# Kernel optimization log

Measured on AMD Instinct MI355X. Metric: run time of the kernel, lower is better.

Reference implementation:

```python
import jax, jax.numpy as jnp
import numpy as np

EPS = 1e-12  # F.normalize eps

def _l2_normalize(x):
    n = jnp.linalg.norm(x, axis=-1, keepdims=True)
    return x / jnp.maximum(n, EPS)

def setup_inputs() -> dict:
    key = jax.random.key(0)
    k1, k2 = jax.random.split(key)
    B, C, F = 32768, 1000, 256
    features = jax.random.normal(k1, (B, F), dtype=jnp.float32)
    prototypes = jax.random.normal(k2, (C, F), dtype=jnp.float32)
    distance_scale = jnp.ones((1,), dtype=jnp.float32)
    temperature = jnp.ones((1,), dtype=jnp.float32)
    return {"features": features, "prototypes": prototypes,
            "distance_scale": distance_scale, "temperature": temperature}

def reference(features, prototypes, distance_scale, temperature):
    # Normalize both sides to the unit sphere (F.normalize, p=2, eps=1e-12)
    fn = _l2_normalize(features)       # [B, F]
    pn = _l2_normalize(prototypes)     # [C, F]
    # For unit vectors: ||a-b||_2 / sqrt(2) = sqrt(1 - a.b)
    cos = jnp.einsum('bf,cf->bc', fn, pn)          # [B, C]
    dist = jnp.sqrt(jnp.maximum(1.0 - cos, 0.0))   # cdist(...)/sqrt(2)
    iso = jnp.abs(distance_scale[0]) * dist
    logits = -(iso + jnp.mean(iso, axis=1, keepdims=True))
    return logits / temperature[0]
```

## Files before the change

### kernel.cpp

```cpp
#include <hip/hip_runtime.h>


typedef __attribute__((ext_vector_type(8))) short short8;
typedef __attribute__((ext_vector_type(4))) float f32x4;
typedef __fp16 h2 __attribute__((ext_vector_type(2)));

union U16 { uint4 u4; short8 s8; };

static __device__ __forceinline__ unsigned short f2bf(float x){
  union { float f; unsigned u; } v; v.f = x;
  unsigned r = v.u + 0x7fffu + ((v.u >> 16) & 1u);
  return (unsigned short)(r >> 16);
}

#define CPAD 1024

__global__ void norm_protos_kernel(const float* __restrict__ src,
                                   unsigned short* __restrict__ dst, int C)
{
  const int wave = threadIdx.x >> 6;
  const int lane = threadIdx.x & 63;
  const int row  = blockIdx.x * 4 + wave;
  const int t    = row >> 4;
  const int l16  = row & 15;
  const int s    = lane >> 3;
  const int quad = (lane >> 1) & 3;
  const int j    = (lane & 1) * 4;

  ushort4 o = {0, 0, 0, 0};
  if (row < C){
    const float4 v = *(const float4*)(src + row * 256 + lane * 4);
    float ss = v.x*v.x + v.y*v.y + v.z*v.z + v.w*v.w;
    #pragma unroll
    for (int off = 32; off; off >>= 1) ss += __shfl_xor(ss, off);
    const float inv = 1.0f / fmaxf(sqrtf(ss), 1e-12f);
    o.x = f2bf(v.x * inv); o.y = f2bf(v.y * inv);
    o.z = f2bf(v.z * inv); o.w = f2bf(v.w * inv);
  }
  *(ushort4*)(dst + ((size_t)((t*8 + s)*64 + quad*16 + l16))*8 + j) = o;
}

__global__ __launch_bounds__(256, 4)
void fused_kernel(const float* __restrict__ feats,
                  const unsigned short* __restrict__ pnw,
                  const float* __restrict__ ds,
                  const float* __restrict__ temp,
                  float* __restrict__ out, int C)
{
  __shared__ float wsum[16][4];

  const int tid  = threadIdx.x;
  const int wave = tid >> 6;
  const int lane = tid & 63;
  const int quad = lane >> 4;
  const int l16  = lane & 15;
  const long rowbase = (long)blockIdx.x * 16;

  short8 ffrag[8];
  {
    const float* rp = feats + (rowbase + l16) * 256 + quad*8;
    float4 va[8], vb[8];
    float ss = 0.f;
    #pragma unroll
    for (int s = 0; s < 8; ++s){
      va[s] = *(const float4*)(rp + s*32);
      vb[s] = *(const float4*)(rp + s*32 + 4);
      ss += va[s].x*va[s].x + va[s].y*va[s].y + va[s].z*va[s].z + va[s].w*va[s].w;
      ss += vb[s].x*vb[s].x + vb[s].y*vb[s].y + vb[s].z*vb[s].z + vb[s].w*vb[s].w;
    }
    ss += __shfl_xor(ss, 16);
    ss += __shfl_xor(ss, 32);
    const float inv = __builtin_amdgcn_rcpf(__builtin_amdgcn_sqrtf(fmaxf(ss, 1e-24f)));
    #pragma unroll
    for (int s = 0; s < 8; ++s){
      U16 u;
      u.u4.x = (unsigned)f2bf(va[s].x*inv) | ((unsigned)f2bf(va[s].y*inv) << 16);
      u.u4.y = (unsigned)f2bf(va[s].z*inv) | ((unsigned)f2bf(va[s].w*inv) << 16);
      u.u4.z = (unsigned)f2bf(vb[s].x*inv) | ((unsigned)f2bf(vb[s].y*inv) << 16);
      u.u4.w = (unsigned)f2bf(vb[s].z*inv) | ((unsigned)f2bf(vb[s].w*inv) << 16);
      ffrag[s] = u.s8;
    }
  }

  const uint4* tp = (const uint4*)pnw + (size_t)(wave*16)*512 + lane;

  h2 dd[16][2];
  float rsum = 0.f;

  #pragma unroll
  for (int wt = 0; wt < 16; ++wt){
    const uint4* bp = tp + (size_t)wt*512;
    short8 pfrag[8];
    #pragma unroll
    for (int s = 0; s < 8; ++s){ U16 u; u.u4 = bp[s*64]; pfrag[s] = u.s8; }

    f32x4 acc = (f32x4){0.f, 0.f, 0.f, 0.f};
    __builtin_amdgcn_s_setprio(1);
    #pragma unroll
    for (int s = 0; s < 8; ++s)
      acc = __builtin_amdgcn_mfma_f32_16x16x32_bf16(pfrag[s], ffrag[s], acc, 0, 0, 0);
    __builtin_amdgcn_s_setprio(0);

    float d0 = __builtin_amdgcn_sqrtf(fmaxf(1.0f - acc[0], 0.0f));
    float d1 = __builtin_amdgcn_sqrtf(fmaxf(1.0f - acc[1], 0.0f));
    float d2 = __builtin_amdgcn_sqrtf(fmaxf(1.0f - acc[2], 0.0f));
    float d3 = __builtin_amdgcn_sqrtf(fmaxf(1.0f - acc[3], 0.0f));

    const int cls = wave*256 + wt*16 + quad*4;
    rsum += (cls < C) ? (d0 + d1 + d2 + d3) : 0.0f;

    dd[wt][0] = __builtin_amdgcn_cvt_pkrtz(d0, d1);
    dd[wt][1] = __builtin_amdgcn_cvt_pkrtz(d2, d3);
  }

  rsum += __shfl_xor(rsum, 16);
  rsum += __shfl_xor(rsum, 32);
  if (quad == 0) wsum[l16][wave] = rsum;
  __syncthreads();

  const float4 wv = *(const float4*)&wsum[l16][0];
  const float mean = (wv.x + wv.y + wv.z + wv.w) / (float)C;
  const float nscale = -fabsf(ds[0]) / temp[0];
  const float bias = nscale * mean;

  float* orow = out + (rowbase + l16) * (size_t)C;
  #pragma unroll
  for (int wt = 0; wt < 16; ++wt){
    const int cls = wave*256 + wt*16 + quad*4;
    if (cls < C){
      f32x4 o;
      o[0] = fmaf(nscale, (float)dd[wt][0][0], bias);
      o[1] = fmaf(nscale, (float)dd[wt][0][1], bias);
      o[2] = fmaf(nscale, (float)dd[wt][1][0], bias);
      o[3] = fmaf(nscale, (float)dd[wt][1][1], bias);
      __builtin_nontemporal_store(o, (f32x4*)(orow + cls));
    }
  }
}

extern "C" void kernel_launch(void* const* d_in, const int* in_sizes, int n_in,
                              void* d_out, int out_size, void* d_ws, size_t ws_size,
                              hipStream_t stream) {
  const float* features = (const float*)d_in[0];
  const float* protos   = (const float*)d_in[1];
  const float* dscale   = (const float*)d_in[2];
  const float* temp     = (const float*)d_in[3];
  float* out = (float*)d_out;

  const int F = 256;
  const int B = in_sizes[0] / F;
  const int C = in_sizes[1] / F;

  unsigned short* pnw = (unsigned short*)d_ws;

  norm_protos_kernel<<<CPAD/4, 256, 0, stream>>>(protos, pnw, C);
  fused_kernel<<<B/16, 256, 0, stream>>>(features, pnw, dscale, temp, out, C);
}
```

Before: 227.7 us.

## Recompute prototype GEMM in output pass instead of caching packed distances

Removes the per-thread fp16-packed distance buffer and instead recomputes the MFMA dot products and sqrt in a second pass after the row mean is known. This cuts register pressure but doubles the matrix work and prototype fragment loads. Launch bounds are lowered to 3 waves per SIMD, outputs are now exact fp32 rather than rounded through fp16, and stores switch from nontemporal to regular.

New measurement: 222.8 us. -2.2%, faster.

```diff
diff --git a/kernel.cpp b/kernel.cpp
--- a/kernel.cpp
+++ b/kernel.cpp
@@ -3,7 +3,6 @@
 
 typedef __attribute__((ext_vector_type(8))) short short8;
 typedef __attribute__((ext_vector_type(4))) float f32x4;
-typedef __fp16 h2 __attribute__((ext_vector_type(2)));
 
 union U16 { uint4 u4; short8 s8; };
 
@@ -40,7 +39,7 @@
   *(ushort4*)(dst + ((size_t)((t*8 + s)*64 + quad*16 + l16))*8 + j) = o;
 }
 
-__global__ __launch_bounds__(256, 4)
+__global__ __launch_bounds__(256, 3)
 void fused_kernel(const float* __restrict__ feats,
                   const unsigned short* __restrict__ pnw,
                   const float* __restrict__ ds,
@@ -83,10 +82,9 @@
   }
 
   const uint4* tp = (const uint4*)pnw + (size_t)(wave*16)*512 + lane;
+  const int cls0 = wave*256 + quad*4;
 
-  h2 dd[16][2];
   float rsum = 0.f;
-
   #pragma unroll
   for (int wt = 0; wt < 16; ++wt){
     const uint4* bp = tp + (size_t)wt*512;
@@ -106,11 +104,7 @@
     float d2 = __builtin_amdgcn_sqrtf(fmaxf(1.0f - acc[2], 0.0f));
     float d3 = __builtin_amdgcn_sqrtf(fmaxf(1.0f - acc[3], 0.0f));
 
-    const int cls = wave*256 + wt*16 + quad*4;
-    rsum += (cls < C) ? (d0 + d1 + d2 + d3) : 0.0f;
-
-    dd[wt][0] = __builtin_amdgcn_cvt_pkrtz(d0, d1);
-    dd[wt][1] = __builtin_amdgcn_cvt_pkrtz(d2, d3);
+    rsum += (cls0 + wt*16 < C) ? (d0 + d1 + d2 + d3) : 0.0f;
   }
 
   rsum += __shfl_xor(rsum, 16);
@@ -126,14 +120,31 @@
   float* orow = out + (rowbase + l16) * (size_t)C;
   #pragma unroll
   for (int wt = 0; wt < 16; ++wt){
-    const int cls = wave*256 + wt*16 + quad*4;
+    const uint4* bp = tp + (size_t)wt*512;
+    short8 pfrag[8];
+    #pragma unroll
+    for (int s = 0; s < 8; ++s){ U16 u; u.u4 = bp[s*64]; pfrag[s] = u.s8; }
+
+    f32x4 acc = (f32x4){0.f, 0.f, 0.f, 0.f};
+    __builtin_amdgcn_s_setprio(1);
+    #pragma unroll
+    for (int s = 0; s < 8; ++s)
+      acc = __builtin_amdgcn_mfma_f32_16x16x32_bf16(pfrag[s], ffrag[s], acc, 0, 0, 0);
+    __builtin_amdgcn_s_setprio(0);
+
+    float d0 = __builtin_amdgcn_sqrtf(fmaxf(1.0f - acc[0], 0.0f));
+    float d1 = __builtin_amdgcn_sqrtf(fmaxf(1.0f - acc[1], 0.0f));
+    float d2 = __builtin_amdgcn_sqrtf(fmaxf(1.0f - acc[2], 0.0f));
+    float d3 = __builtin_amdgcn_sqrtf(fmaxf(1.0f - acc[3], 0.0f));
+
+    const int cls = cls0 + wt*16;
     if (cls < C){
-      f32x4 o;
-      o[0] = fmaf(nscale, (float)dd[wt][0][0], bias);
-      o[1] = fmaf(nscale, (float)dd[wt][0][1], bias);
-      o[2] = fmaf(nscale, (float)dd[wt][1][0], bias);
-      o[3] = fmaf(nscale, (float)dd[wt][1][1], bias);
-      __builtin_nontemporal_store(o, (f32x4*)(orow + cls));
+      float4 o;
+      o.x = fmaf(nscale, d0, bias);
+      o.y = fmaf(nscale, d1, bias);
+      o.z = fmaf(nscale, d2, bias);
+      o.w = fmaf(nscale, d3, bias);
+      *(float4*)(orow + cls) = o;
     }
   }
 }
```

## Split into bias and store passes with 64-row tiles and LDS-staged prototypes

Applied to the files above, without the earlier changes.

The single fused kernel is replaced by two passes that both recompute the GEMM. The first pass only computes per-row mean distances into a workspace buffer. The second recomputes the distances and writes the final logits directly, so the fp16 register buffering of all distances is no longer needed. Each block now handles 64 rows, reusing each prototype fragment across four MFMAs, and prototype tiles are double-buffered into LDS with async global_load_lds. The cost is a second full pass over features and the matmul, plus one extra launch and a small workspace write and read.

Result: slower. 232.5 us (+2.1%).

```diff
diff --git a/kernel.cpp b/kernel.cpp
--- a/kernel.cpp
+++ b/kernel.cpp
@@ -3,7 +3,6 @@
 
 typedef __attribute__((ext_vector_type(8))) short short8;
 typedef __attribute__((ext_vector_type(4))) float f32x4;
-typedef __fp16 h2 __attribute__((ext_vector_type(2)));
 
 union U16 { uint4 u4; short8 s8; };
 
@@ -40,100 +39,230 @@
   *(ushort4*)(dst + ((size_t)((t*8 + s)*64 + quad*16 + l16))*8 + j) = o;
 }
 
-__global__ __launch_bounds__(256, 4)
-void fused_kernel(const float* __restrict__ feats,
-                  const unsigned short* __restrict__ pnw,
-                  const float* __restrict__ ds,
-                  const float* __restrict__ temp,
-                  float* __restrict__ out, int C)
+#define VMWAIT8 do{ asm volatile("s_waitcnt vmcnt(8)" ::: "memory"); \
+                    __builtin_amdgcn_sched_barrier(0); }while(0)
+#define VMWAIT0 do{ asm volatile("s_waitcnt vmcnt(0)" ::: "memory"); \
+                    __builtin_amdgcn_sched_barrier(0); }while(0)
+
+static __device__ __forceinline__ void stage_tile(const uint4* g, uint4* l){
+  #pragma unroll
+  for (int s = 0; s < 8; ++s)
+    __builtin_amdgcn_global_load_lds(
+      (const __attribute__((address_space(1))) void*)(g + s*64),
+      (__attribute__((address_space(3))) void*)(l + s*64), 16, 0, 0);
+}
+
+static __device__ __forceinline__ void load_ffrag(const float* rp, short8* fr){
+  float4 va[8], vb[8];
+  float ss = 0.f;
+  #pragma unroll
+  for (int s = 0; s < 8; ++s){
+    va[s] = *(const float4*)(rp + s*32);
+    vb[s] = *(const float4*)(rp + s*32 + 4);
+    ss += va[s].x*va[s].x + va[s].y*va[s].y + va[s].z*va[s].z + va[s].w*va[s].w;
+    ss += vb[s].x*vb[s].x + vb[s].y*vb[s].y + vb[s].z*vb[s].z + vb[s].w*vb[s].w;
+  }
+  ss += __shfl_xor(ss, 16);
+  ss += __shfl_xor(ss, 32);
+  const float inv = __builtin_amdgcn_rcpf(__builtin_amdgcn_sqrtf(fmaxf(ss, 1e-24f)));
+  #pragma unroll
+  for (int s = 0; s < 8; ++s){
+    U16 u;
+    u.u4.x = (unsigned)f2bf(va[s].x*inv) | ((unsigned)f2bf(va[s].y*inv) << 16);
+    u.u4.y = (unsigned)f2bf(va[s].z*inv) | ((unsigned)f2bf(va[s].w*inv) << 16);
+    u.u4.z = (unsigned)f2bf(vb[s].x*inv) | ((unsigned)f2bf(vb[s].y*inv) << 16);
+    u.u4.w = (unsigned)f2bf(vb[s].z*inv) | ((unsigned)f2bf(vb[s].w*inv) << 16);
+    fr[s] = u.s8;
+  }
+}
+
+__global__ __launch_bounds__(256, 2)
+void bias_kernel(const float* __restrict__ feats,
+                 const unsigned short* __restrict__ pnw,
+                 const float* __restrict__ ds,
+                 const float* __restrict__ temp,
+                 float* __restrict__ rowbias, int C)
 {
-  __shared__ float wsum[16][4];
+  __shared__ uint4 pring[4][2][512];
+  __shared__ float wsum[4][16][4];
 
   const int tid  = threadIdx.x;
   const int wave = tid >> 6;
   const int lane = tid & 63;
   const int quad = lane >> 4;
   const int l16  = lane & 15;
-  const long rowbase = (long)blockIdx.x * 16;
-
-  short8 ffrag[8];
-  {
-    const float* rp = feats + (rowbase + l16) * 256 + quad*8;
-    float4 va[8], vb[8];
-    float ss = 0.f;
+  const long rowbase = (long)blockIdx.x * 64;
+
+  short8 ffrag[4][8];
+  #pragma unroll
+  for (int rg = 0; rg < 4; ++rg)
+    load_ffrag(feats + (rowbase + rg*16 + l16) * 256 + quad*8, ffrag[rg]);
+
+  const uint4* tpg = (const uint4*)pnw + (size_t)(wave*16)*512 + lane;
+  uint4* ringp = &pring[wave][0][0];
+
+  __builtin_amdgcn_sched_barrier(0);
+  stage_tile(tpg,       ringp);
+  stage_tile(tpg + 512, ringp + 512);
+
+  float rs0 = 0.f, rs1 = 0.f, rs2 = 0.f, rs3 = 0.f;
+
+  #pragma unroll
+  for (int wt = 0; wt < 16; ++wt){
+    if (wt < 15) { VMWAIT8; } else { VMWAIT0; }
+
+    const uint4* l = ringp + (wt & 1)*512;
+    short8 pfrag[8];
+    #pragma unroll
+    for (int s = 0; s < 8; ++s){ U16 u; u.u4 = l[s*64 + lane]; pfrag[s] = u.s8; }
+
+    f32x4 a0 = (f32x4){0,0,0,0}, a1 = (f32x4){0,0,0,0};
+    f32x4 a2 = (f32x4){0,0,0,0}, a3 = (f32x4){0,0,0,0};
+    __builtin_amdgcn_s_setprio(1);
     #pragma unroll
     for (int s = 0; s < 8; ++s){
-      va[s] = *(const float4*)(rp + s*32);
-      vb[s] = *(const float4*)(rp + s*32 + 4);
-      ss += va[s].x*va[s].x + va[s].y*va[s].y + va[s].z*va[s].z + va[s].w*va[s].w;
-      ss += vb[s].x*vb[s].x + vb[s].y*vb[s].y + vb[s].z*vb[s].z + vb[s].w*vb[s].w;
-    }
-    ss += __shfl_xor(ss, 16);
-    ss += __shfl_xor(ss, 32);
-    const float inv = __builtin_amdgcn_rcpf(__builtin_amdgcn_sqrtf(fmaxf(ss, 1e-24f)));
-    #pragma unroll
-    for (int s = 0; s < 8; ++s){
-      U16 u;
-      u.u4.x = (unsigned)f2bf(va[s].x*inv) | ((unsigned)f2bf(va[s].y*inv) << 16);
-      u.u4.y = (unsigned)f2bf(va[s].z*inv) | ((unsigned)f2bf(va[s].w*inv) << 16);
-      u.u4.z = (unsigned)f2bf(vb[s].x*inv) | ((unsigned)f2bf(vb[s].y*inv) << 16);
-      u.u4.w = (unsigned)f2bf(vb[s].z*inv) | ((unsigned)f2bf(vb[s].w*inv) << 16);
-      ffrag[s] = u.s8;
-    }
-  }
-
-  const uint4* tp = (const uint4*)pnw + (size_t)(wave*16)*512 + lane;
-
-  h2 dd[16][2];
-  float rsum = 0.f;
-
-  #pragma unroll
-  for (int wt = 0; wt < 16; ++wt){
-    const uint4* bp = tp + (size_t)wt*512;
-    short8 pfrag[8];
-    #pragma unroll
-    for (int s = 0; s < 8; ++s){ U16 u; u.u4 = bp[s*64]; pfrag[s] = u.s8; }
-
-    f32x4 acc = (f32x4){0.f, 0.f, 0.f, 0.f};
-    __builtin_amdgcn_s_setprio(1);
-    #pragma unroll
-    for (int s = 0; s < 8; ++s)
-      acc = __builtin_amdgcn_mfma_f32_16x16x32_bf16(pfrag[s], ffrag[s], acc, 0, 0, 0);
+      a0 = __builtin_amdgcn_mfma_f32_16x16x32_bf16(pfrag[s], ffrag[0][s], a0, 0, 0, 0);
+      a1 = __builtin_amdgcn_mfma_f32_16x16x32_bf16(pfrag[s], ffrag[1][s], a1, 0, 0, 0);
+      a2 = __builtin_amdgcn_mfma_f32_16x16x32_bf16(pfrag[s], ffrag[2][s], a2, 0, 0, 0);
+      a3 = __builtin_amdgcn_mfma_f32_16x16x32_bf16(pfrag[s], ffrag[3][s], a3, 0, 0, 0);
+    }
     __builtin_amdgcn_s_setprio(0);
 
-    float d0 = __builtin_amdgcn_sqrtf(fmaxf(1.0f - acc[0], 0.0f));
-    float d1 = __builtin_amdgcn_sqrtf(fmaxf(1.0f - acc[1], 0.0f));
-    float d2 = __builtin_amdgcn_sqrtf(fmaxf(1.0f - acc[2], 0.0f));
-    float d3 = __builtin_amdgcn_sqrtf(fmaxf(1.0f - acc[3], 0.0f));
-
-    const int cls = wave*256 + wt*16 + quad*4;
-    rsum += (cls < C) ? (d0 + d1 + d2 + d3) : 0.0f;
-
-    dd[wt][0] = __builtin_amdgcn_cvt_pkrtz(d0, d1);
-    dd[wt][1] = __builtin_amdgcn_cvt_pkrtz(d2, d3);
-  }
-
-  rsum += __shfl_xor(rsum, 16);
-  rsum += __shfl_xor(rsum, 32);
-  if (quad == 0) wsum[l16][wave] = rsum;
-  __syncthreads();
-
-  const float4 wv = *(const float4*)&wsum[l16][0];
-  const float mean = (wv.x + wv.y + wv.z + wv.w) / (float)C;
-  const float nscale = -fabsf(ds[0]) / temp[0];
-  const float bias = nscale * mean;
-
-  float* orow = out + (rowbase + l16) * (size_t)C;
-  #pragma unroll
-  for (int wt = 0; wt < 16; ++wt){
+    if (wt + 2 < 16){
+      __builtin_amdgcn_sched_barrier(0);
+      stage_tile(tpg + (size_t)(wt + 2)*512, ringp + (wt & 1)*512);
+    }
+
     const int cls = wave*256 + wt*16 + quad*4;
     if (cls < C){
-      f32x4 o;
-      o[0] = fmaf(nscale, (float)dd[wt][0][0], bias);
-      o[1] = fmaf(nscale, (float)dd[wt][0][1], bias);
-      o[2] = fmaf(nscale, (float)dd[wt][1][0], bias);
-      o[3] = fmaf(nscale, (float)dd[wt][1][1], bias);
-      __builtin_nontemporal_store(o, (f32x4*)(orow + cls));
+      rs0 += __builtin_amdgcn_sqrtf(fmaxf(1.0f - a0[0], 0.0f))
+           + __builtin_amdgcn_sqrtf(fmaxf(1.0f - a0[1], 0.0f))
+           + __builtin_amdgcn_sqrtf(fmaxf(1.0f - a0[2], 0.0f))
+           + __builtin_amdgcn_sqrtf(fmaxf(1.0f - a0[3], 0.0f));
+      rs1 += __builtin_amdgcn_sqrtf(fmaxf(1.0f - a1[0], 0.0f))
+           + __builtin_amdgcn_sqrtf(fmaxf(1.0f - a1[1], 0.0f))
+           + __builtin_amdgcn_sqrtf(fmaxf(1.0f - a1[2], 0.0f))
+           + __builtin_amdgcn_sqrtf(fmaxf(1.0f - a1[3], 0.0f));
+      rs2 += __builtin_amdgcn_sqrtf(fmaxf(1.0f - a2[0], 0.0f))
+           + __builtin_amdgcn_sqrtf(fmaxf(1.0f - a2[1], 0.0f))
+           + __builtin_amdgcn_sqrtf(fmaxf(1.0f - a2[2], 0.0f))
+           + __builtin_amdgcn_sqrtf(fmaxf(1.0f - a2[3], 0.0f));
+      rs3 += __builtin_amdgcn_sqrtf(fmaxf(1.0f - a3[0], 0.0f))
+           + __builtin_amdgcn_sqrtf(fmaxf(1.0f - a3[1], 0.0f))
+           + __builtin_amdgcn_sqrtf(fmaxf(1.0f - a3[2], 0.0f))
+           + __builtin_amdgcn_sqrtf(fmaxf(1.0f - a3[3], 0.0f));
+    }
+  }
+
+  rs0 += __shfl_xor(rs0, 16); rs0 += __shfl_xor(rs0, 32);
+  rs1 += __shfl_xor(rs1, 16); rs1 += __shfl_xor(rs1, 32);
+  rs2 += __shfl_xor(rs2, 16); rs2 += __shfl_xor(rs2, 32);
+  rs3 += __shfl_xor(rs3, 16); rs3 += __shfl_xor(rs3, 32);
+  if (quad == 0){
+    wsum[0][l16][wave] = rs0;
+    wsum[1][l16][wave] = rs1;
+    wsum[2][l16][wave] = rs2;
+    wsum[3][l16][wave] = rs3;
+  }
+  __syncthreads();
+
+  if (tid < 64){
+    const float4 w = *(const float4*)&wsum[tid >> 4][tid & 15][0];
+    const float mean = (w.x + w.y + w.z + w.w) / (float)C;
+    const float nscale = -fabsf(ds[0]) / temp[0];
+    rowbias[rowbase + tid] = nscale * mean;
+  }
+}
+
+__global__ __launch_bounds__(256, 2)
+void store_kernel(const float* __restrict__ feats,
+                  const unsigned short* __restrict__ pnw,
+                  const float* __restrict__ rowbias,
+                  const float* __restrict__ ds,
+                  const float* __restrict__ temp,
+                  float* __restrict__ out, int C)
+{
+  __shared__ uint4 pring[4][2][512];
+
+  const int tid  = threadIdx.x;
+  const int wave = tid >> 6;
+  const int lane = tid & 63;
+  const int quad = lane >> 4;
+  const int l16  = lane & 15;
+  const long rowbase = (long)blockIdx.x * 64;
+
+  short8 ffrag[4][8];
+  #pragma unroll
+  for (int rg = 0; rg < 4; ++rg)
+    load_ffrag(feats + (rowbase + rg*16 + l16) * 256 + quad*8, ffrag[rg]);
+
+  const float nscale = -fabsf(ds[0]) / temp[0];
+  const float bias0 = rowbias[rowbase      + l16];
+  const float bias1 = rowbias[rowbase + 16 + l16];
+  const float bias2 = rowbias[rowbase + 32 + l16];
+  const float bias3 = rowbias[rowbase + 48 + l16];
+
+  float* orow0 = out + (rowbase      + l16) * (size_t)C;
+  float* orow1 = out + (rowbase + 16 + l16) * (size_t)C;
+  float* orow2 = out + (rowbase + 32 + l16) * (size_t)C;
+  float* orow3 = out + (rowbase + 48 + l16) * (size_t)C;
+
+  const uint4* tpg = (const uint4*)pnw + (size_t)(wave*16)*512 + lane;
+  uint4* ringp = &pring[wave][0][0];
+
+  __builtin_amdgcn_sched_barrier(0);
+  stage_tile(tpg,       ringp);
+  stage_tile(tpg + 512, ringp + 512);
+
+  #pragma unroll
+  for (int wt = 0; wt < 16; ++wt){
+    if (wt < 15) { VMWAIT8; } else { VMWAIT0; }
+
+    const uint4* l = ringp + (wt & 1)*512;
+    short8 pfrag[8];
+    #pragma unroll
+    for (int s = 0; s < 8; ++s){ U16 u; u.u4 = l[s*64 + lane]; pfrag[s] = u.s8; }
+
+    f32x4 a0 = (f32x4){0,0,0,0}, a1 = (f32x4){0,0,0,0};
+    f32x4 a2 = (f32x4){0,0,0,0}, a3 = (f32x4){0,0,0,0};
+    __builtin_amdgcn_s_setprio(1);
+    #pragma unroll
+    for (int s = 0; s < 8; ++s){
+      a0 = __builtin_amdgcn_mfma_f32_16x16x32_bf16(pfrag[s], ffrag[0][s], a0, 0, 0, 0);
+      a1 = __builtin_amdgcn_mfma_f32_16x16x32_bf16(pfrag[s], ffrag[1][s], a1, 0, 0, 0);
+      a2 = __builtin_amdgcn_mfma_f32_16x16x32_bf16(pfrag[s], ffrag[2][s], a2, 0, 0, 0);
+      a3 = __builtin_amdgcn_mfma_f32_16x16x32_bf16(pfrag[s], ffrag[3][s], a3, 0, 0, 0);
+    }
+    __builtin_amdgcn_s_setprio(0);
+
+    if (wt + 2 < 16){
+      __builtin_amdgcn_sched_barrier(0);
+      stage_tile(tpg + (size_t)(wt + 2)*512, ringp + (wt & 1)*512);
+    }
+
+    const int cls = wave*256 + wt*16 + quad*4;
+    if (cls < C){
+      float4 o;
+      o.x = fmaf(nscale, __builtin_amdgcn_sqrtf(fmaxf(1.0f - a0[0], 0.0f)), bias0);
+      o.y = fmaf(nscale, __builtin_amdgcn_sqrtf(fmaxf(1.0f - a0[1], 0.0f)), bias0);
+      o.z = fmaf(nscale, __builtin_amdgcn_sqrtf(fmaxf(1.0f - a0[2], 0.0f)), bias0);
+      o.w = fmaf(nscale, __builtin_amdgcn_sqrtf(fmaxf(1.0f - a0[3], 0.0f)), bias0);
+      *(float4*)(orow0 + cls) = o;
+      o.x = fmaf(nscale, __builtin_amdgcn_sqrtf(fmaxf(1.0f - a1[0], 0.0f)), bias1);
+      o.y = fmaf(nscale, __builtin_amdgcn_sqrtf(fmaxf(1.0f - a1[1], 0.0f)), bias1);
+      o.z = fmaf(nscale, __builtin_amdgcn_sqrtf(fmaxf(1.0f - a1[2], 0.0f)), bias1);
+      o.w = fmaf(nscale, __builtin_amdgcn_sqrtf(fmaxf(1.0f - a1[3], 0.0f)), bias1);
+      *(float4*)(orow1 + cls) = o;
+      o.x = fmaf(nscale, __builtin_amdgcn_sqrtf(fmaxf(1.0f - a2[0], 0.0f)), bias2);
+      o.y = fmaf(nscale, __builtin_amdgcn_sqrtf(fmaxf(1.0f - a2[1], 0.0f)), bias2);
+      o.z = fmaf(nscale, __builtin_amdgcn_sqrtf(fmaxf(1.0f - a2[2], 0.0f)), bias2);
+      o.w = fmaf(nscale, __builtin_amdgcn_sqrtf(fmaxf(1.0f - a2[3], 0.0f)), bias2);
+      *(float4*)(orow2 + cls) = o;
+      o.x = fmaf(nscale, __builtin_amdgcn_sqrtf(fmaxf(1.0f - a3[0], 0.0f)), bias3);
+      o.y = fmaf(nscale, __builtin_amdgcn_sqrtf(fmaxf(1.0f - a3[1], 0.0f)), bias3);
+      o.z = fmaf(nscale, __builtin_amdgcn_sqrtf(fmaxf(1.0f - a3[2], 0.0f)), bias3);
+      o.w = fmaf(nscale, __builtin_amdgcn_sqrtf(fmaxf(1.0f - a3[3], 0.0f)), bias3);
+      *(float4*)(orow3 + cls) = o;
     }
   }
 }
@@ -152,7 +281,9 @@
   const int C = in_sizes[1] / F;
 
   unsigned short* pnw = (unsigned short*)d_ws;
+  float* rowbias = (float*)((char*)d_ws + CPAD*256*2);
 
   norm_protos_kernel<<<CPAD/4, 256, 0, stream>>>(protos, pnw, C);
-  fused_kernel<<<B/16, 256, 0, stream>>>(features, pnw, dscale, temp, out, C);
-}
+  bias_kernel<<<B/64, 256, 0, stream>>>(features, pnw, dscale, temp, rowbias, C);
+  store_kernel<<<B/64, 256, 0, stream>>>(features, pnw, rowbias, dscale, temp, out, C);
+}
```
